# Optimization experiments

Measured on AMD Instinct MI355X. Metric: run time of the kernel, lower is better.

The kernel has to match this reference:

```python
import jax, jax.numpy as jnp
import numpy as np

D_MODEL, D_STATE, B, S = 1024, 64, 8, 2048


def setup_inputs() -> dict:
    key = jax.random.key(0)
    ks = jax.random.split(key, 14)
    inp = {"x": jax.random.normal(ks[0], (B, S, D_MODEL), jnp.float32)}
    names = ["cog", "beh", "env", "delta", "Bp", "Cp"]
    for i, n in enumerate(names):
        inp[f"W_{n}"] = jax.random.normal(ks[1 + 2 * i], (D_STATE, D_MODEL), jnp.float32) / np.sqrt(D_MODEL)
        inp[f"b_{n}"] = jnp.zeros((D_STATE,), jnp.float32)
    # torch init is log(|randn|+1e-4); we use strictly-negative A_log so the
    # length-2048 multiplicative recurrence stays finite (A_log is a learned
    # parameter, so its value is free; the math of forward is unchanged).
    inp["A_log"] = -jnp.abs(jax.random.normal(ks[13], (D_STATE, D_STATE), jnp.float32)) - 0.1
    return inp


def reference(x, W_cog, b_cog, W_beh, b_beh, W_env, b_env,
              W_delta, b_delta, W_Bp, b_Bp, W_Cp, b_Cp, A_log):
    # gating terms (computed in the source but never used downstream)
    A_t = (jax.nn.sigmoid(x @ W_cog.T + b_cog)
           * jax.nn.sigmoid(x @ W_beh.T + b_beh)
           * jax.nn.sigmoid(x @ W_env.T + b_env))
    del A_t

    delta = jax.nn.softplus(x @ W_delta.T + b_delta)   # [B,S,N]
    Bt = x @ W_Bp.T + b_Bp                             # [B,S,N]
    Ct = x @ W_Cp.T + b_Cp                             # [B,S,N]
    u = Bt * x[:, :, :D_STATE]                         # [B,S,N]

    # Faithful to torch broadcasting: after step 0 the carried state h is
    # [B,N,N] with h[b,i,j] = exp(A_log[i,j]*delta[b,t,i]) * h_prev[b,i,j] + u[b,t,j]
    def step(h, td):
        d, u_t, c_t = td                               # each [B,N]
        A = jnp.exp(A_log[None, :, :] * d[:, :, None]) # [B,N,N]
        h = A * h + u_t[:, None, :]
        y = jnp.einsum('bj,bij->bi', c_t, h)           # [B,N]
        return h, y

    h0 = jnp.zeros((x.shape[0], D_STATE, D_STATE), x.dtype)
    _, ys = jax.lax.scan(
        step, h0,
        (delta.transpose(1, 0, 2), u.transpose(1, 0, 2), Ct.transpose(1, 0, 2)))
    # torch stacks y_t of shape [B,1,N] along dim=1 -> [B,S,1,N]
    return ys.transpose(1, 0, 2)[:, :, None, :]
```

## Files before the change

### kernel.cpp

```cpp
#include <hip/hip_runtime.h>
#include <math.h>

#define DM   1024
#define DS   64
#define BATCH 8
#define SEQ  2048
#define CL   32
#define NC   64

typedef __bf16 bf16x8 __attribute__((ext_vector_type(8)));
typedef __bf16 bf16x4 __attribute__((ext_vector_type(4)));
typedef float  f32x4  __attribute__((ext_vector_type(4)));

__global__ __launch_bounds__(256) void wconv_kernel(
    const float* __restrict__ Wd, const float* __restrict__ Wb,
    const float* __restrict__ Wc, __bf16* __restrict__ Wp)
{
    int idx = blockIdx.x * 256 + threadIdx.x;
    int k  = idx & 1023;
    int n  = idx >> 10;
    const float* W = (n < 64) ? Wd : (n < 128 ? Wb : Wc);
    float v = W[(size_t)(n & 63) * DM + k];
    int kt = k >> 5, kk = k & 31;
    Wp[((size_t)kt * 192 + n) * 32 + kk] = (__bf16)v;
}

__global__ __launch_bounds__(256) void proj_mfma(
    const float* __restrict__ x, const __bf16* __restrict__ Wp,
    const float* __restrict__ bd, const float* __restrict__ bb,
    const float* __restrict__ bc,
    float* __restrict__ delta_g, float* __restrict__ u_g,
    float* __restrict__ ct_g)
{
    __shared__ __bf16 sAh[32 * 40];
    __shared__ __bf16 sAl[32 * 40];
    __shared__ __bf16 sB[192 * 40];

    const int tid  = threadIdx.x;
    const int row0 = blockIdx.x * 32;

    const int sx_row = tid >> 3;
    const int sx_sub = tid & 7;
    const float* xg = x + (size_t)(row0 + sx_row) * DM + sx_sub * 4;
    const int wn0  = tid >> 2;
    const int wsub = tid & 3;

    const int lane = tid & 63, wv = tid >> 6;
    const int l15 = lane & 15, quad = lane >> 4;
    const int mrow  = (wv & 1) * 16;
    const int nbase = (wv >> 1) * 96;

    f32x4 acc[6];
    #pragma unroll
    for (int i = 0; i < 6; ++i) acc[i] = (f32x4){0.f, 0.f, 0.f, 0.f};

    float4 xA, xB;
    uint4 wA0, wA1, wA2, wB0, wB1, wB2;

    #define LOADX(dst, kt)  dst = *(const float4*)(xg + (kt) * 32)
    #define LOADW(d0, d1, d2, kt) do {                                        \
        const __bf16* wp = Wp + ((size_t)(kt) * 192) * 32 + wsub * 8;         \
        d0 = *(const uint4*)(wp + (size_t)(wn0      ) * 32);                  \
        d1 = *(const uint4*)(wp + (size_t)(wn0 +  64) * 32);                  \
        d2 = *(const uint4*)(wp + (size_t)(wn0 + 128) * 32);                  \
    } while (0)

    #define STAGE(xc, w0, w1, w2) do {                                        \
        __bf16 h0 = (__bf16)xc.x, h1 = (__bf16)xc.y,                          \
               h2 = (__bf16)xc.z, h3 = (__bf16)xc.w;                          \
        bf16x4 hv = {h0, h1, h2, h3};                                         \
        bf16x4 lv = {(__bf16)(xc.x - (float)h0), (__bf16)(xc.y - (float)h1),  \
                     (__bf16)(xc.z - (float)h2), (__bf16)(xc.w - (float)h3)}; \
        *(bf16x4*)&sAh[sx_row * 40 + sx_sub * 4] = hv;                        \
        *(bf16x4*)&sAl[sx_row * 40 + sx_sub * 4] = lv;                        \
        *(uint4*)&sB[(wn0      ) * 40 + wsub * 8] = w0;                       \
        *(uint4*)&sB[(wn0 +  64) * 40 + wsub * 8] = w1;                       \
        *(uint4*)&sB[(wn0 + 128) * 40 + wsub * 8] = w2;                       \
    } while (0)

    #define COMPUTE() do {                                                    \
        bf16x8 ah = *(const bf16x8*)&sAh[(mrow + l15) * 40 + quad * 8];       \
        bf16x8 al = *(const bf16x8*)&sAl[(mrow + l15) * 40 + quad * 8];       \
        _Pragma("unroll")                                                     \
        for (int nt = 0; nt < 6; ++nt) {                                      \
            bf16x8 bf = *(const bf16x8*)                                      \
                &sB[(nbase + nt * 16 + l15) * 40 + quad * 8];                 \
            acc[nt] = __builtin_amdgcn_mfma_f32_16x16x32_bf16(                \
                ah, bf, acc[nt], 0, 0, 0);                                    \
            acc[nt] = __builtin_amdgcn_mfma_f32_16x16x32_bf16(                \
                al, bf, acc[nt], 0, 0, 0);                                    \
        }                                                                     \
    } while (0)

    LOADX(xA, 0);
    LOADW(wA0, wA1, wA2, 0);

    for (int kt = 0; kt < 32; kt += 2) {
        LOADX(xB, kt + 1);
        LOADW(wB0, wB1, wB2, kt + 1);
        STAGE(xA, wA0, wA1, wA2);
        __syncthreads();
        COMPUTE();
        __syncthreads();
        if (kt + 2 < 32) {
            LOADX(xA, kt + 2);
            LOADW(wA0, wA1, wA2, kt + 2);
        }
        STAGE(xB, wB0, wB1, wB2);
        __syncthreads();
        COMPUTE();
        __syncthreads();
    }

    #pragma unroll
    for (int nt = 0; nt < 6; ++nt) {
        int gn  = nbase + nt * 16 + l15;
        int mat = gn >> 6;
        int col = gn & 63;
        float bias = (mat == 0) ? bd[col] : (mat == 1 ? bb[col] : bc[col]);
        #pragma unroll
        for (int r = 0; r < 4; ++r) {
            int m = row0 + mrow + quad * 4 + r;
            float v = acc[nt][r] + bias;
            if (mat == 0) {
                float sp = (v > 20.f) ? v : log1pf(__expf(v));
                delta_g[(size_t)m * DS + col] = sp;
            } else if (mat == 1) {
                u_g[(size_t)m * DS + col] = v * x[(size_t)m * DM + col];
            } else {
                ct_g[(size_t)m * DS + col] = v;
            }
        }
    }
    #undef LOADX
    #undef LOADW
    #undef STAGE
    #undef COMPUTE
}

__global__ __launch_bounds__(256) void pass1_kernel(
    const float* __restrict__ delta_g, const float* __restrict__ u_g,
    const float* __restrict__ A_log,
    float* __restrict__ E, float* __restrict__ Dsum)
{
    __shared__ float s_d[CL * 64];
    __shared__ float s_u[CL * 64];
    const int c = blockIdx.x, b = blockIdx.y, tid = threadIdx.x;
    const int t0 = c * CL;

    const float4* dg = (const float4*)(delta_g + ((size_t)b * SEQ + t0) * DS);
    const float4* ug = (const float4*)(u_g     + ((size_t)b * SEQ + t0) * DS);
    #pragma unroll
    for (int it = 0; it < (CL * 64 / 4) / 256; ++it) {
        int f = tid + it * 256;
        ((float4*)s_d)[f] = dg[f];
        ((float4*)s_u)[f] = ug[f];
    }

    const int i  = tid & 63;
    const int jg = tid >> 6;
    float alog[16];
    {
        const float4* ar = (const float4*)(A_log + i * 64 + jg * 16);
        #pragma unroll
        for (int q = 0; q < 4; ++q) {
            float4 v = ar[q];
            alog[4*q+0] = v.x; alog[4*q+1] = v.y;
            alog[4*q+2] = v.z; alog[4*q+3] = v.w;
        }
    }
    __syncthreads();

    float h[16];
    #pragma unroll
    for (int k = 0; k < 16; ++k) h[k] = 0.f;
    float dsum = 0.f;

    for (int t = 0; t < CL; ++t) {
        float d = s_d[t * 64 + i];
        dsum += d;
        const float* up = s_u + t * 64 + jg * 16;
        #pragma unroll
        for (int k = 0; k < 16; ++k)
            h[k] = __expf(alog[k] * d) * h[k] + up[k];
    }

    float* eo = E + (((size_t)c * BATCH + b) * 64 + i) * 64 + jg * 16;
    #pragma unroll
    for (int q = 0; q < 4; ++q)
        ((float4*)eo)[q] = make_float4(h[4*q], h[4*q+1], h[4*q+2], h[4*q+3]);
    if (jg == 0) Dsum[((size_t)c * BATCH + b) * 64 + i] = dsum;
}

__global__ __launch_bounds__(256) void pass2_kernel(
    const float* __restrict__ A_log, const float* __restrict__ E,
    const float* __restrict__ Dsum, float* __restrict__ Sin)
{
    const int g = blockIdx.x * 256 + threadIdx.x;
    const int b = g >> 12;
    const int e = g & 4095;
    const int i = e >> 6;
    const float al = A_log[e];
    float carry = 0.f;
    for (int c = 0; c < NC; ++c) {
        const size_t base = ((size_t)c * BATCH + b) * 4096;
        Sin[base + e] = carry;
        carry = __expf(al * Dsum[((size_t)c * BATCH + b) * 64 + i]) * carry
                + E[base + e];
    }
}

__global__ __launch_bounds__(256) void pass3_kernel(
    const float* __restrict__ delta_g, const float* __restrict__ u_g,
    const float* __restrict__ ct_g, const float* __restrict__ A_log,
    const float* __restrict__ Sin, float* __restrict__ out)
{
    __shared__ float s_d[CL * 64];
    __shared__ float s_u[CL * 64];
    __shared__ float s_c[CL * 64];
    __shared__ float ypart[2][4][64];

    const int c = blockIdx.x, b = blockIdx.y, tid = threadIdx.x;
    const int t0 = c * CL;

    const float4* dg = (const float4*)(delta_g + ((size_t)b * SEQ + t0) * DS);
    const float4* ug = (const float4*)(u_g     + ((size_t)b * SEQ + t0) * DS);
    const float4* cg = (const float4*)(ct_g    + ((size_t)b * SEQ + t0) * DS);
    #pragma unroll
    for (int it = 0; it < (CL * 64 / 4) / 256; ++it) {
        int f = tid + it * 256;
        ((float4*)s_d)[f] = dg[f];
        ((float4*)s_u)[f] = ug[f];
        ((float4*)s_c)[f] = cg[f];
    }

    const int i  = tid & 63;
    const int jg = tid >> 6;
    float alog[16];
    {
        const float4* ar = (const float4*)(A_log + i * 64 + jg * 16);
        #pragma unroll
        for (int q = 0; q < 4; ++q) {
            float4 v = ar[q];
            alog[4*q+0] = v.x; alog[4*q+1] = v.y;
            alog[4*q+2] = v.z; alog[4*q+3] = v.w;
        }
    }

    float h[16];
    {
        const float4* hin = (const float4*)(
            Sin + (((size_t)c * BATCH + b) * 64 + i) * 64 + jg * 16);
        #pragma unroll
        for (int q = 0; q < 4; ++q) {
            float4 v = hin[q];
            h[4*q+0] = v.x; h[4*q+1] = v.y; h[4*q+2] = v.z; h[4*q+3] = v.w;
        }
    }
    __syncthreads();

    int buf = 0;
    for (int t = 0; t < CL; ++t) {
        float d = s_d[t * 64 + i];
        const float* up = s_u + t * 64 + jg * 16;
        const float* cp = s_c + t * 64 + jg * 16;
        float part = 0.f;
        #pragma unroll
        for (int k = 0; k < 16; ++k) {
            h[k] = __expf(alog[k] * d) * h[k] + up[k];
            part += cp[k] * h[k];
        }
        ypart[buf][jg][i] = part;
        __syncthreads();
        if (tid < 64) {
            float y = ypart[buf][0][tid] + ypart[buf][1][tid]
                    + ypart[buf][2][tid] + ypart[buf][3][tid];
            out[((size_t)b * SEQ + t0 + t) * DS + tid] = y;
        }
        buf ^= 1;
    }
}

extern "C" void kernel_launch(void* const* d_in, const int* in_sizes, int n_in,
                              void* d_out, int out_size, void* d_ws, size_t ws_size,
                              hipStream_t stream)
{
    const float* x     = (const float*)d_in[0];
    const float* Wd    = (const float*)d_in[7];
    const float* bd    = (const float*)d_in[8];
    const float* Wb    = (const float*)d_in[9];
    const float* bb    = (const float*)d_in[10];
    const float* Wc    = (const float*)d_in[11];
    const float* bc    = (const float*)d_in[12];
    const float* A_log = (const float*)d_in[13];
    float* out = (float*)d_out;

    float* ws = (float*)d_ws;
    float* delta_g = ws;
    float* u_g     = ws + 1 * 1048576;
    float* ct_g    = ws + 2 * 1048576;
    float* E       = ws + 3 * 1048576;
    float* Sin     = ws + 5 * 1048576;
    float* Dsum    = ws + 7 * 1048576;
    __bf16* Wp     = (__bf16*)E;

    wconv_kernel<<<768, 256, 0, stream>>>(Wd, Wb, Wc, Wp);
    proj_mfma<<<512, 256, 0, stream>>>(
        x, Wp, bd, bb, bc, delta_g, u_g, ct_g);
    pass1_kernel<<<dim3(NC, BATCH), 256, 0, stream>>>(
        delta_g, u_g, A_log, E, Dsum);
    pass2_kernel<<<(BATCH * 4096) / 256, 256, 0, stream>>>(
        A_log, E, Dsum, Sin);
    pass3_kernel<<<dim3(NC, BATCH), 256, 0, stream>>>(
        delta_g, u_g, ct_g, A_log, Sin, out);
}
```

Before: 192.3 us.

## Drop bf16 split-precision GEMM, double-buffer LDS, prefetch pass2, shuffle-reduce pass3

The projection GEMM no longer splits x into high and low bf16 parts, so half the MFMAs and the low-part LDS traffic are gone. It also switches to a double-buffered LDS pipeline with one barrier per k-tile. pass2 prefetches E and the decay factors four chunks ahead, and pass3 remaps threads so the four j-groups of a row reduce with wavefront shuffles instead of a per-step LDS barrier. Dropping the low bf16 part lowers the precision of delta, u and Ct, which the length-2048 recurrence may amplify.

```diff
diff --git a/kernel.cpp b/kernel.cpp
--- a/kernel.cpp
+++ b/kernel.cpp
@@ -32,9 +32,8 @@
     float* __restrict__ delta_g, float* __restrict__ u_g,
     float* __restrict__ ct_g)
 {
-    __shared__ __bf16 sAh[32 * 40];
-    __shared__ __bf16 sAl[32 * 40];
-    __shared__ __bf16 sB[192 * 40];
+    __shared__ __bf16 sA[2][32 * 40];
+    __shared__ __bf16 sB[2][192 * 40];
 
     const int tid  = threadIdx.x;
     const int row0 = blockIdx.x * 32;
@@ -54,62 +53,47 @@
     #pragma unroll
     for (int i = 0; i < 6; ++i) acc[i] = (f32x4){0.f, 0.f, 0.f, 0.f};
 
-    float4 xA, xB;
-    uint4 wA0, wA1, wA2, wB0, wB1, wB2;
-
-    #define LOADX(dst, kt)  dst = *(const float4*)(xg + (kt) * 32)
-    #define LOADW(d0, d1, d2, kt) do {                                        \
+    float4 xr;
+    uint4 w0, w1, w2;
+
+    #define LOAD(kt) do {                                                     \
+        xr = *(const float4*)(xg + (kt) * 32);                                \
         const __bf16* wp = Wp + ((size_t)(kt) * 192) * 32 + wsub * 8;         \
-        d0 = *(const uint4*)(wp + (size_t)(wn0      ) * 32);                  \
-        d1 = *(const uint4*)(wp + (size_t)(wn0 +  64) * 32);                  \
-        d2 = *(const uint4*)(wp + (size_t)(wn0 + 128) * 32);                  \
+        w0 = *(const uint4*)(wp + (size_t)(wn0      ) * 32);                  \
+        w1 = *(const uint4*)(wp + (size_t)(wn0 +  64) * 32);                  \
+        w2 = *(const uint4*)(wp + (size_t)(wn0 + 128) * 32);                  \
     } while (0)
 
-    #define STAGE(xc, w0, w1, w2) do {                                        \
-        __bf16 h0 = (__bf16)xc.x, h1 = (__bf16)xc.y,                          \
-               h2 = (__bf16)xc.z, h3 = (__bf16)xc.w;                          \
-        bf16x4 hv = {h0, h1, h2, h3};                                         \
-        bf16x4 lv = {(__bf16)(xc.x - (float)h0), (__bf16)(xc.y - (float)h1),  \
-                     (__bf16)(xc.z - (float)h2), (__bf16)(xc.w - (float)h3)}; \
-        *(bf16x4*)&sAh[sx_row * 40 + sx_sub * 4] = hv;                        \
-        *(bf16x4*)&sAl[sx_row * 40 + sx_sub * 4] = lv;                        \
-        *(uint4*)&sB[(wn0      ) * 40 + wsub * 8] = w0;                       \
-        *(uint4*)&sB[(wn0 +  64) * 40 + wsub * 8] = w1;                       \
-        *(uint4*)&sB[(wn0 + 128) * 40 + wsub * 8] = w2;                       \
+    #define STAGE(bi) do {                                                    \
+        bf16x4 hv = {(__bf16)xr.x, (__bf16)xr.y, (__bf16)xr.z, (__bf16)xr.w}; \
+        *(bf16x4*)&sA[bi][sx_row * 40 + sx_sub * 4] = hv;                     \
+        *(uint4*)&sB[bi][(wn0      ) * 40 + wsub * 8] = w0;                   \
+        *(uint4*)&sB[bi][(wn0 +  64) * 40 + wsub * 8] = w1;                   \
+        *(uint4*)&sB[bi][(wn0 + 128) * 40 + wsub * 8] = w2;                   \
     } while (0)
 
-    #define COMPUTE() do {                                                    \
-        bf16x8 ah = *(const bf16x8*)&sAh[(mrow + l15) * 40 + quad * 8];       \
-        bf16x8 al = *(const bf16x8*)&sAl[(mrow + l15) * 40 + quad * 8];       \
+    #define COMPUTE(bi) do {                                                  \
+        bf16x8 ah = *(const bf16x8*)&sA[bi][(mrow + l15) * 40 + quad * 8];    \
         _Pragma("unroll")                                                     \
         for (int nt = 0; nt < 6; ++nt) {                                      \
             bf16x8 bf = *(const bf16x8*)                                      \
-                &sB[(nbase + nt * 16 + l15) * 40 + quad * 8];                 \
+                &sB[bi][(nbase + nt * 16 + l15) * 40 + quad * 8];             \
             acc[nt] = __builtin_amdgcn_mfma_f32_16x16x32_bf16(                \
                 ah, bf, acc[nt], 0, 0, 0);                                    \
-            acc[nt] = __builtin_amdgcn_mfma_f32_16x16x32_bf16(                \
-                al, bf, acc[nt], 0, 0, 0);                                    \
         }                                                                     \
     } while (0)
 
-    LOADX(xA, 0);
-    LOADW(wA0, wA1, wA2, 0);
-
-    for (int kt = 0; kt < 32; kt += 2) {
-        LOADX(xB, kt + 1);
-        LOADW(wB0, wB1, wB2, kt + 1);
-        STAGE(xA, wA0, wA1, wA2);
+    LOAD(0);
+    STAGE(0);
+    __syncthreads();
+
+    int buf = 0;
+    for (int kt = 0; kt < 32; ++kt) {
+        if (kt < 31) LOAD(kt + 1);
+        COMPUTE(buf);
+        if (kt < 31) STAGE(buf ^ 1);
         __syncthreads();
-        COMPUTE();
-        __syncthreads();
-        if (kt + 2 < 32) {
-            LOADX(xA, kt + 2);
-            LOADW(wA0, wA1, wA2, kt + 2);
-        }
-        STAGE(xB, wB0, wB1, wB2);
-        __syncthreads();
-        COMPUTE();
-        __syncthreads();
+        buf ^= 1;
     }
 
     #pragma unroll
@@ -132,8 +116,7 @@
             }
         }
     }
-    #undef LOADX
-    #undef LOADW
+    #undef LOAD
     #undef STAGE
     #undef COMPUTE
 }
@@ -201,12 +184,27 @@
     const int e = g & 4095;
     const int i = e >> 6;
     const float al = A_log[e];
+
+    float Eb[4], db[4];
+    #pragma unroll
+    for (int p = 0; p < 4; ++p) {
+        size_t nb = (size_t)p * BATCH + b;
+        Eb[p] = E[nb * 4096 + e];
+        db[p] = __expf(al * Dsum[nb * 64 + i]);
+    }
+
     float carry = 0.f;
+    #pragma unroll 4
     for (int c = 0; c < NC; ++c) {
-        const size_t base = ((size_t)c * BATCH + b) * 4096;
-        Sin[base + e] = carry;
-        carry = __expf(al * Dsum[((size_t)c * BATCH + b) * 64 + i]) * carry
-                + E[base + e];
+        const int s = c & 3;
+        float Ec = Eb[s], dc = db[s];
+        if (c + 4 < NC) {
+            size_t nb = (size_t)(c + 4) * BATCH + b;
+            Eb[s] = E[nb * 4096 + e];
+            db[s] = __expf(al * Dsum[nb * 64 + i]);
+        }
+        Sin[((size_t)c * BATCH + b) * 4096 + e] = carry;
+        carry = dc * carry + Ec;
     }
 }
 
@@ -218,7 +216,6 @@
     __shared__ float s_d[CL * 64];
     __shared__ float s_u[CL * 64];
     __shared__ float s_c[CL * 64];
-    __shared__ float ypart[2][4][64];
 
     const int c = blockIdx.x, b = blockIdx.y, tid = threadIdx.x;
     const int t0 = c * CL;
@@ -234,8 +231,9 @@
         ((float4*)s_c)[f] = cg[f];
     }
 
-    const int i  = tid & 63;
-    const int jg = tid >> 6;
+    const int i  = tid >> 2;
+    const int jg = tid & 3;
+
     float alog[16];
     {
         const float4* ar = (const float4*)(A_log + i * 64 + jg * 16);
@@ -259,7 +257,6 @@
     }
     __syncthreads();
 
-    int buf = 0;
     for (int t = 0; t < CL; ++t) {
         float d = s_d[t * 64 + i];
         const float* up = s_u + t * 64 + jg * 16;
@@ -270,14 +267,10 @@
             h[k] = __expf(alog[k] * d) * h[k] + up[k];
             part += cp[k] * h[k];
         }
-        ypart[buf][jg][i] = part;
-        __syncthreads();
-        if (tid < 64) {
-            float y = ypart[buf][0][tid] + ypart[buf][1][tid]
-                    + ypart[buf][2][tid] + ypart[buf][3][tid];
-            out[((size_t)b * SEQ + t0 + t) * DS + tid] = y;
-        }
-        buf ^= 1;
+        part += __shfl_xor(part, 1);
+        part += __shfl_xor(part, 2);
+        if (jg == 0)
+            out[((size_t)b * SEQ + t0 + t) * DS + i] = part;
     }
 }
 
```

Result: slower. 204.2 us (+6.2%).
